# Kernel optimization log

Measured on AMD Instinct MI355X. Metric: run time of the kernel, lower is better.

Reference implementation:

```python
import jax, jax.numpy as jnp
import numpy as np

N = 100000
E = 3200000
F_IN, F1, F2, F3, FB, NC = 256, 64, 32, 16, 8, 10


def setup_inputs() -> dict:
    key = jax.random.key(0)
    ks = jax.random.split(key, 12)
    features = jax.random.normal(ks[0], (N, F_IN), dtype=jnp.float32)
    edge_index = jax.random.randint(ks[1], (2, E), 0, N, dtype=jnp.int64)
    def glorot(k, shape):
        lim = np.sqrt(6.0 / (shape[0] + shape[1]))
        return jax.random.uniform(k, shape, jnp.float32, -lim, lim)
    return {
        "features": features,
        "edge_index": edge_index,
        "W1": glorot(ks[2], (F_IN, F1)), "b1": jnp.zeros((F1,), jnp.float32),
        "W2": glorot(ks[3], (F1, F2)),  "b2": jnp.zeros((F2,), jnp.float32),
        "W3": glorot(ks[4], (F2, F3)),  "b3": jnp.zeros((F3,), jnp.float32),
        "Wf": glorot(ks[5], (F3, FB)),  "bf": jnp.zeros((FB,), jnp.float32),
        "Ws": glorot(ks[6], (FB, NC)),  "bs": jnp.zeros((NC,), jnp.float32),
    }


def _gcn_norm(edge_index, n):
    # symmetric normalization with self-loops: deg includes +1 for self-loop
    src, dst = edge_index[0], edge_index[1]
    ones = jnp.ones((edge_index.shape[1],), jnp.float32)
    deg = jax.ops.segment_sum(ones, dst, num_segments=n) + 1.0
    dinv = jax.lax.rsqrt(deg)
    edge_w = dinv[src] * dinv[dst]        # [E]
    self_w = dinv * dinv                   # [N], self-loop weight
    return src, dst, edge_w, self_w


def _gcn_conv(x, W, b, src, dst, edge_w, self_w, n):
    xw = x @ W                                         # [N, Fout]
    msg = xw[src] * edge_w[:, None]                    # gather + scale
    agg = jax.ops.segment_sum(msg, dst, num_segments=n)
    return agg + xw * self_w[:, None] + b


def reference(features, edge_index, W1, b1, W2, b2, W3, b3, Wf, bf, Ws, bs):
    n = features.shape[0]
    src, dst, edge_w, self_w = _gcn_norm(edge_index, n)
    h = jax.nn.relu(_gcn_conv(features, W1, b1, src, dst, edge_w, self_w, n))
    h = jax.nn.relu(_gcn_conv(h, W2, b2, src, dst, edge_w, self_w, n))
    h = jax.nn.relu(_gcn_conv(h, W3, b3, src, dst, edge_w, self_w, n))
    pooled = jnp.mean(h, axis=0, keepdims=True)        # [1, F3]
    hidden = jax.nn.relu(pooled @ Wf + bf)
    scores = hidden @ Ws + bs
    return jax.nn.log_softmax(scores, axis=1)
```

## Files before the change

### kernel.cpp

```cpp
#include <hip/hip_runtime.h>
#include <hip/hip_fp16.h>
#include <math.h>

#define TPB 256
#define BKT_SHIFT 9
#define BKT_N 512
#define NB_MAX 256
#define CHUNK 4096
#define CAP   24576
#define Y_SCALE 16.0f
#define Y_INV_SCALE (1.0f / 16.0f)

typedef short bf16x8 __attribute__((ext_vector_type(8)));
typedef float f32x4  __attribute__((ext_vector_type(4)));

static __device__ inline unsigned short f2bf(float f) {
    union { float f; unsigned u; } v; v.f = f;
    unsigned r = v.u + 0x7FFF + ((v.u >> 16) & 1);
    return (unsigned short)(r >> 16);
}

static __device__ inline unsigned char f2fp8(float x) {
    int p = __builtin_amdgcn_cvt_pk_fp8_f32(x, x, 0, false);
    return (unsigned char)(p & 0xFF);
}

static __device__ inline void acc_word(float* a, unsigned u) {
    a[0] += __builtin_amdgcn_cvt_f32_fp8(u, 0);
    a[1] += __builtin_amdgcn_cvt_f32_fp8(u, 1);
    a[2] += __builtin_amdgcn_cvt_f32_fp8(u, 2);
    a[3] += __builtin_amdgcn_cvt_f32_fp8(u, 3);
}

__global__ __launch_bounds__(256) void init_cursor(int* __restrict__ bcursor, int nbkt) {
    int t = threadIdx.x;
    if (t < nbkt) bcursor[t] = t * CAP;
}

__global__ __launch_bounds__(TPB) void bucket_scatter(
    const int* __restrict__ src, const int* __restrict__ dst,
    int* __restrict__ bcursor, unsigned int* __restrict__ packed, int E, int nbkt)
{
    __shared__ unsigned int  spk[CHUNK];
    __shared__ unsigned char sbk[CHUNK];
    __shared__ int h[NB_MAX];
    __shared__ int base[NB_MAX];
    for (int c0 = blockIdx.x * CHUNK; c0 < E; c0 += gridDim.x * CHUNK) {
        int m = min(CHUNK, E - c0);
        for (int i = threadIdx.x; i < nbkt; i += TPB) h[i] = 0;
        __syncthreads();
        for (int i = threadIdx.x; i < m; i += TPB) {
            int d = dst[c0 + i];
            int s = src[c0 + i];
            int b = d >> BKT_SHIFT;
            spk[i] = ((unsigned)(d & (BKT_N - 1)) << 17) | (unsigned)s;
            sbk[i] = (unsigned char)b;
            atomicAdd(&h[b], 1);
        }
        __syncthreads();
        for (int i = threadIdx.x; i < nbkt; i += TPB) {
            int c = h[i];
            base[i] = c ? atomicAdd(&bcursor[i], c) : 0;
            h[i] = 0;
        }
        __syncthreads();
        for (int i = threadIdx.x; i < m; i += TPB) {
            int b = sbk[i];
            int pos = base[b] + atomicAdd(&h[b], 1);
            packed[pos] = spk[i];
        }
        __syncthreads();
    }
}

__global__ __launch_bounds__(256) void bucket_offsets(
    const int* __restrict__ bcursor, int* __restrict__ boff, int nbkt, int E)
{
    int t = threadIdx.x;
    int v = (t < nbkt) ? (bcursor[t] - t * CAP) : 0;
    __shared__ int tmp[256];
    tmp[t] = v; __syncthreads();
    for (int s = 1; s < 256; s <<= 1) {
        int x = (t >= s) ? tmp[t - s] : 0;
        __syncthreads();
        tmp[t] += x;
        __syncthreads();
    }
    if (t < nbkt) boff[t] = tmp[t] - v;
    if (t == 0) boff[nbkt] = E;
}

__global__ __launch_bounds__(256) void bucket_csr(
    const unsigned int* __restrict__ packed, const int* __restrict__ boff,
    int* __restrict__ off, float* __restrict__ dinv, int* __restrict__ ssrc,
    int n, int nbkt)
{
    const int b   = blockIdx.x;
    const int e0  = boff[b];
    const int cnt = boff[b + 1] - e0;
    const int p0  = b * CAP;
    const int v0  = b << BKT_SHIFT;
    const int nv  = min(BKT_N, n - v0);
    const int t   = threadIdx.x;

    __shared__ int hist[BKT_N];
    __shared__ int cur[BKT_N];
    __shared__ int tmp[256];

    for (int i = t; i < nv; i += 256) hist[i] = 0;
    __syncthreads();
    for (int e = t; e < cnt; e += 256)
        atomicAdd(&hist[packed[p0 + e] >> 17], 1);
    __syncthreads();

    int a = (2 * t     < nv) ? hist[2 * t]     : 0;
    int c = (2 * t + 1 < nv) ? hist[2 * t + 1] : 0;
    int ps = a + c;
    tmp[t] = ps; __syncthreads();
    for (int s = 1; s < 256; s <<= 1) {
        int x = (t >= s) ? tmp[t - s] : 0;
        __syncthreads();
        tmp[t] += x;
        __syncthreads();
    }
    int ex = tmp[t] - ps;
    if (2 * t < nv) {
        cur[2 * t] = ex;
        off[v0 + 2 * t] = e0 + ex;
        dinv[v0 + 2 * t] = rsqrtf((float)a + 1.0f);
    }
    if (2 * t + 1 < nv) {
        cur[2 * t + 1] = ex + a;
        off[v0 + 2 * t + 1] = e0 + ex + a;
        dinv[v0 + 2 * t + 1] = rsqrtf((float)c + 1.0f);
    }
    if (b == nbkt - 1 && t == 0) off[n] = boff[nbkt];
    __syncthreads();

    for (int e = t; e < cnt; e += 256) {
        unsigned p = packed[p0 + e];
        int dl = p >> 17;
        int s  = p & 0x1FFFF;
        int pos = atomicAdd(&cur[dl], 1);
        ssrc[e0 + pos] = s;
    }
}

__global__ __launch_bounds__(256) void conv_w(
    const float* __restrict__ W, unsigned short* __restrict__ Wt, int K, int N)
{
    int total = K * N;
    for (int i = threadIdx.x + blockIdx.x * 256; i < total; i += gridDim.x * 256) {
        int k = i / N, c = i % N;
        Wt[c * K + k] = f2bf(W[i]);
    }
}

template<int K, int NCOL, typename AT>
__global__ __launch_bounds__(TPB) void gemm_mfma(
    const AT* __restrict__ A, const unsigned short* __restrict__ Wt,
    const float* __restrict__ dinv, unsigned char* __restrict__ Yq, int n)
{
    constexpr int NT = NCOL / 16;
    constexpr int KS = K / 32;
    const int lane = threadIdx.x & 63;
    const int w    = threadIdx.x >> 6;
    const int rowbase = blockIdx.x * 128 + w * 32;
    const int arow = lane & 15;
    const int kb   = (lane >> 4) * 8;

    f32x4 acc[2][NT];
#pragma unroll
    for (int mt = 0; mt < 2; mt++)
#pragma unroll
        for (int nt = 0; nt < NT; nt++) acc[mt][nt] = (f32x4)(0.f);

#pragma unroll
    for (int ks = 0; ks < KS; ks++) {
        bf16x8 a[2];
#pragma unroll
        for (int mt = 0; mt < 2; mt++) {
            int r = rowbase + mt * 16 + arow;
            if constexpr (sizeof(AT) == 4) {
                if (r < n) {
                    const float4* p = (const float4*)(A + (size_t)r * K + ks * 32 + kb);
                    float4 u = p[0], v = p[1];
                    a[mt][0] = f2bf(u.x); a[mt][1] = f2bf(u.y);
                    a[mt][2] = f2bf(u.z); a[mt][3] = f2bf(u.w);
                    a[mt][4] = f2bf(v.x); a[mt][5] = f2bf(v.y);
                    a[mt][6] = f2bf(v.z); a[mt][7] = f2bf(v.w);
                } else {
#pragma unroll
                    for (int i = 0; i < 8; i++) a[mt][i] = 0;
                }
            } else {
                if (r < n)
                    a[mt] = *(const bf16x8*)(A + (size_t)r * K + ks * 32 + kb);
                else {
#pragma unroll
                    for (int i = 0; i < 8; i++) a[mt][i] = 0;
                }
            }
        }
        bf16x8 b[NT];
#pragma unroll
        for (int nt = 0; nt < NT; nt++)
            b[nt] = *(const bf16x8*)(Wt + (size_t)(nt * 16 + arow) * K + ks * 32 + kb);
#pragma unroll
        for (int mt = 0; mt < 2; mt++)
#pragma unroll
            for (int nt = 0; nt < NT; nt++)
                acc[mt][nt] = __builtin_amdgcn_mfma_f32_16x16x32_bf16(
                    a[mt], b[nt], acc[mt][nt], 0, 0, 0);
    }

#pragma unroll
    for (int mt = 0; mt < 2; mt++) {
        int r0 = rowbase + mt * 16 + (lane >> 4) * 4;
#pragma unroll
        for (int j = 0; j < 4; j++) {
            int r = r0 + j;
            if (r < n) {
                float dv = dinv[r] * Y_SCALE;
#pragma unroll
                for (int nt = 0; nt < NT; nt++)
                    Yq[(size_t)r * NCOL + nt * 16 + arow] = f2fp8(acc[mt][nt][j] * dv);
            }
        }
    }
}

template<int F>
__global__ __launch_bounds__(TPB) void seg_group(
    const int* __restrict__ off, const int* __restrict__ ssrc,
    const unsigned char* __restrict__ Yq, const float* __restrict__ dinv,
    const float* __restrict__ bias, unsigned int* __restrict__ H, int n)
{
    constexpr int G     = F / 16;
    constexpr int LOG2G = (G == 4) ? 2 : 1;
    const int lane  = threadIdx.x & 63;
    const int fl    = lane & (G - 1);
    const int gbase = lane & ~(G - 1);
    const int v     = (blockIdx.x * TPB + threadIdx.x) >> LOG2G;

    if (v >= n) return;

    float acc[16];
#pragma unroll
    for (int i = 0; i < 16; i++) acc[i] = 0.f;

    {
        uint4 q = *(const uint4*)(Yq + (size_t)v * F + fl * 16);
        acc_word(acc + 0, q.x); acc_word(acc + 4, q.y);
        acc_word(acc + 8, q.z); acc_word(acc + 12, q.w);
    }

    const int e0 = off[v], e1 = off[v + 1];
    int e = e0;
    for (; e + G <= e1; e += G) {
        int idx = ssrc[e + fl];
        uint4 q[G];
#pragma unroll
        for (int k = 0; k < G; k++) {
            int sj = __shfl(idx, gbase + k, 64);
            q[k] = *(const uint4*)(Yq + (size_t)sj * F + fl * 16);
        }
#pragma unroll
        for (int k = 0; k < G; k++) {
            acc_word(acc + 0, q[k].x); acc_word(acc + 4, q[k].y);
            acc_word(acc + 8, q[k].z); acc_word(acc + 12, q[k].w);
        }
    }
    int rem = e1 - e;
    if (rem > 0) {
        int idx = (fl < rem) ? ssrc[e + fl] : 0;
        for (int k = 0; k < rem; k++) {
            int sj = __shfl(idx, gbase + k, 64);
            uint4 q = *(const uint4*)(Yq + (size_t)sj * F + fl * 16);
            acc_word(acc + 0, q.x); acc_word(acc + 4, q.y);
            acc_word(acc + 8, q.z); acc_word(acc + 12, q.w);
        }
    }

    float dv = dinv[v] * Y_INV_SCALE;
    unsigned hw[8];
#pragma unroll
    for (int i = 0; i < 16; i += 2) {
        float rx = fmaxf(fmaf(acc[i],     dv, bias[fl * 16 + i]),     0.f);
        float ry = fmaxf(fmaf(acc[i + 1], dv, bias[fl * 16 + i + 1]), 0.f);
        hw[i / 2] = ((unsigned)f2bf(ry) << 16) | (unsigned)f2bf(rx);
    }
    unsigned int* hp = H + (size_t)v * (F / 2) + fl * 8;
    *(uint4*)(hp + 0) = make_uint4(hw[0], hw[1], hw[2], hw[3]);
    *(uint4*)(hp + 4) = make_uint4(hw[4], hw[5], hw[6], hw[7]);
}

__global__ __launch_bounds__(TPB) void seg_pool16(
    const int* __restrict__ off, const int* __restrict__ ssrc,
    const unsigned char* __restrict__ Yq, const float* __restrict__ dinv,
    const float* __restrict__ bias, float* __restrict__ pooled, int n)
{
    constexpr int U = 4;
    const int v = blockIdx.x * TPB + threadIdx.x;

    float r16[16];
#pragma unroll
    for (int i = 0; i < 16; i++) r16[i] = 0.f;

    if (v < n) {
        float acc[16];
#pragma unroll
        for (int i = 0; i < 16; i++) acc[i] = 0.f;

        {
            uint4 q = *(const uint4*)(Yq + (size_t)v * 16);
            acc_word(acc + 0, q.x); acc_word(acc + 4, q.y);
            acc_word(acc + 8, q.z); acc_word(acc + 12, q.w);
        }
        int e0 = off[v], e1 = off[v + 1];
        int e = e0;
        for (; e + U <= e1; e += U) {
            uint4 q[U];
#pragma unroll
            for (int k = 0; k < U; k++)
                q[k] = *(const uint4*)(Yq + (size_t)ssrc[e + k] * 16);
#pragma unroll
            for (int k = 0; k < U; k++) {
                acc_word(acc + 0, q[k].x); acc_word(acc + 4, q[k].y);
                acc_word(acc + 8, q[k].z); acc_word(acc + 12, q[k].w);
            }
        }
        for (; e < e1; e++) {
            uint4 q = *(const uint4*)(Yq + (size_t)ssrc[e] * 16);
            acc_word(acc + 0, q.x); acc_word(acc + 4, q.y);
            acc_word(acc + 8, q.z); acc_word(acc + 12, q.w);
        }

        float dv = dinv[v] * Y_INV_SCALE;
#pragma unroll
        for (int i = 0; i < 16; i++)
            r16[i] = fmaxf(fmaf(acc[i], dv, bias[i]), 0.f);
    }

    __shared__ float red[TPB][17];
#pragma unroll
    for (int i = 0; i < 16; i++) red[threadIdx.x][i] = r16[i];
    __syncthreads();
    for (int st = 128; st >= 1; st >>= 1) {
        if (threadIdx.x < st) {
#pragma unroll
            for (int i = 0; i < 16; i++)
                red[threadIdx.x][i] += red[threadIdx.x + st][i];
        }
        __syncthreads();
    }
    if (threadIdx.x < 16) atomicAdd(&pooled[threadIdx.x], red[0][threadIdx.x]);
}

__global__ void head_kernel(const float* __restrict__ pooled,
                            const float* __restrict__ Wf, const float* __restrict__ bf,
                            const float* __restrict__ Ws, const float* __restrict__ bs,
                            float* __restrict__ out, float invn)
{
    if (threadIdx.x == 0 && blockIdx.x == 0) {
        float p[16], h[8], s[10];
        for (int i = 0; i < 16; i++) p[i] = pooled[i] * invn;
        for (int j = 0; j < 8; j++) {
            float a = bf[j];
            for (int i = 0; i < 16; i++) a = fmaf(p[i], Wf[i * 8 + j], a);
            h[j] = fmaxf(a, 0.f);
        }
        float m = -1e30f;
        for (int c = 0; c < 10; c++) {
            float a = bs[c];
            for (int j = 0; j < 8; j++) a = fmaf(h[j], Ws[j * 10 + c], a);
            s[c] = a;
            m = fmaxf(m, a);
        }
        float lse = 0.f;
        for (int c = 0; c < 10; c++) lse += expf(s[c] - m);
        lse = logf(lse) + m;
        for (int c = 0; c < 10; c++) out[c] = s[c] - lse;
    }
}

static inline size_t align_up(size_t x) { return (x + 255) & ~(size_t)255; }

extern "C" void kernel_launch(void* const* d_in, const int* in_sizes, int n_in,
                              void* d_out, int out_size, void* d_ws, size_t ws_size,
                              hipStream_t stream)
{
    const float* X  = (const float*)d_in[0];
    const int*   ei = (const int*)  d_in[1];
    const float* W1 = (const float*)d_in[2];  const float* b1 = (const float*)d_in[3];
    const float* W2 = (const float*)d_in[4];  const float* b2 = (const float*)d_in[5];
    const float* W3 = (const float*)d_in[6];  const float* b3 = (const float*)d_in[7];
    const float* Wf = (const float*)d_in[8];  const float* bf = (const float*)d_in[9];
    const float* Ws = (const float*)d_in[10]; const float* bs = (const float*)d_in[11];

    const int n = in_sizes[0] / 256;
    const int E = in_sizes[1] / 2;
    const int* src = ei;
    const int* dst = ei + E;
    const int nbkt = (n + BKT_N - 1) / BKT_N;

    char* ws = (char*)d_ws;
    size_t off_b = 0;
    int* bcursor = (int*)(ws + off_b);   off_b += align_up(NB_MAX * 4);
    int* boff    = (int*)(ws + off_b);   off_b += align_up((NB_MAX + 1) * 4);
    float* dinv  = (float*)(ws + off_b); off_b += align_up((size_t)n * 4);
    int* off     = (int*)(ws + off_b);   off_b += align_up((size_t)(n + 1) * 4);
    float* pooled= (float*)(ws + off_b); off_b += align_up(16 * 4);
    unsigned short* Wt1 = (unsigned short*)(ws + off_b); off_b += align_up(64 * 256 * 2);
    unsigned short* Wt2 = (unsigned short*)(ws + off_b); off_b += align_up(32 * 64 * 2);
    unsigned short* Wt3 = (unsigned short*)(ws + off_b); off_b += align_up(16 * 32 * 2);
    unsigned int* packed = (unsigned int*)(ws + off_b); off_b += align_up((size_t)nbkt * CAP * 4);
    int* ssrc    = (int*)(ws + off_b);   off_b += align_up((size_t)E * 4);
    unsigned char* Yq = (unsigned char*)(ws + off_b); off_b += align_up((size_t)n * 64);
    unsigned int* H = (unsigned int*)(ws + off_b); off_b += align_up((size_t)n * 64 * 2);

    hipMemsetAsync(pooled, 0, 16 * 4, stream);

    init_cursor<<<1, 256, 0, stream>>>(bcursor, nbkt);
    int nchunk = (E + CHUNK - 1) / CHUNK;
    bucket_scatter<<<nchunk, TPB, 0, stream>>>(src, dst, bcursor, packed, E, nbkt);
    bucket_offsets<<<1, 256, 0, stream>>>(bcursor, boff, nbkt, E);
    bucket_csr<<<nbkt, 256, 0, stream>>>(packed, boff, off, dinv, ssrc, n, nbkt);

    conv_w<<<16, 256, 0, stream>>>(W1, Wt1, 256, 64);
    conv_w<<<2, 256, 0, stream>>>(W2, Wt2, 64, 32);
    conv_w<<<1, 256, 0, stream>>>(W3, Wt3, 32, 16);

    const int gblk = (n + 127) / 128;
    const int nblk = (n + TPB - 1) / TPB;

    gemm_mfma<256, 64, float><<<gblk, TPB, 0, stream>>>(X, Wt1, dinv, Yq, n);
    seg_group<64><<<(4 * n + TPB - 1) / TPB, TPB, 0, stream>>>(off, ssrc, Yq, dinv, b1, H, n);

    gemm_mfma<64, 32, unsigned short><<<gblk, TPB, 0, stream>>>(
        (const unsigned short*)H, Wt2, dinv, Yq, n);
    seg_group<32><<<(2 * n + TPB - 1) / TPB, TPB, 0, stream>>>(off, ssrc, Yq, dinv, b2, H, n);

    gemm_mfma<32, 16, unsigned short><<<gblk, TPB, 0, stream>>>(
        (const unsigned short*)H, Wt3, dinv, Yq, n);
    seg_pool16<<<nblk, TPB, 0, stream>>>(off, ssrc, Yq, dinv, b3, pooled, n);

    head_kernel<<<1, 64, 0, stream>>>(pooled, Wf, bf, Ws, bs, (float*)d_out, 1.0f / (float)n);
}
```

Baseline: 265.0 us.

## Split layer-1 fp8 features into two column halves and aggregate each separately

The first GEMM now writes its 64-column fp8 output as two planar 32-byte-per-row halves, and the layer-1 aggregation runs as two passes of a 2-lane-per-node kernel, one per half, each writing into its slice of H. Each gather pass touches a 3.2 MB table instead of a 6.4 MB one, aiming for better cache hit rates on the random source gathers. The cost is reading the CSR offsets and indices twice plus an extra launch. The bucket-scatter chunk size is also halved.

Result: slower. 303.7 us (+14.6%).

```diff
diff --git a/kernel.cpp b/kernel.cpp
--- a/kernel.cpp
+++ b/kernel.cpp
@@ -6,7 +6,7 @@
 #define BKT_SHIFT 9
 #define BKT_N 512
 #define NB_MAX 256
-#define CHUNK 4096
+#define CHUNK 2048
 #define CAP   24576
 #define Y_SCALE 16.0f
 #define Y_INV_SCALE (1.0f / 16.0f)
@@ -222,26 +222,31 @@
             int r = r0 + j;
             if (r < n) {
                 float dv = dinv[r] * Y_SCALE;
-#pragma unroll
-                for (int nt = 0; nt < NT; nt++)
-                    Yq[(size_t)r * NCOL + nt * 16 + arow] = f2fp8(acc[mt][nt][j] * dv);
+                if constexpr (NCOL == 64) {
+#pragma unroll
+                    for (int nt = 0; nt < NT; nt++)
+                        Yq[(size_t)(nt >> 1) * n * 32 + (size_t)r * 32 +
+                           (nt & 1) * 16 + arow] = f2fp8(acc[mt][nt][j] * dv);
+                } else {
+#pragma unroll
+                    for (int nt = 0; nt < NT; nt++)
+                        Yq[(size_t)r * NCOL + nt * 16 + arow] = f2fp8(acc[mt][nt][j] * dv);
+                }
             }
         }
     }
 }
 
-template<int F>
-__global__ __launch_bounds__(TPB) void seg_group(
+template<int HSTRIDE>
+__global__ __launch_bounds__(TPB) void seg_group32(
     const int* __restrict__ off, const int* __restrict__ ssrc,
-    const unsigned char* __restrict__ Yq, const float* __restrict__ dinv,
-    const float* __restrict__ bias, unsigned int* __restrict__ H, int n)
-{
-    constexpr int G     = F / 16;
-    constexpr int LOG2G = (G == 4) ? 2 : 1;
+    const unsigned char* __restrict__ yb, const float* __restrict__ dinv,
+    const float* __restrict__ bias, unsigned int* __restrict__ H, int hoff, int n)
+{
     const int lane  = threadIdx.x & 63;
-    const int fl    = lane & (G - 1);
-    const int gbase = lane & ~(G - 1);
-    const int v     = (blockIdx.x * TPB + threadIdx.x) >> LOG2G;
+    const int fl    = lane & 1;
+    const int gbase = lane & ~1;
+    const int v     = (blockIdx.x * TPB + threadIdx.x) >> 1;
 
     if (v >= n) return;
 
@@ -250,36 +255,30 @@
     for (int i = 0; i < 16; i++) acc[i] = 0.f;
 
     {
-        uint4 q = *(const uint4*)(Yq + (size_t)v * F + fl * 16);
+        uint4 q = *(const uint4*)(yb + (size_t)v * 32 + fl * 16);
         acc_word(acc + 0, q.x); acc_word(acc + 4, q.y);
         acc_word(acc + 8, q.z); acc_word(acc + 12, q.w);
     }
 
     const int e0 = off[v], e1 = off[v + 1];
     int e = e0;
-    for (; e + G <= e1; e += G) {
+    for (; e + 2 <= e1; e += 2) {
         int idx = ssrc[e + fl];
-        uint4 q[G];
-#pragma unroll
-        for (int k = 0; k < G; k++) {
-            int sj = __shfl(idx, gbase + k, 64);
-            q[k] = *(const uint4*)(Yq + (size_t)sj * F + fl * 16);
-        }
-#pragma unroll
-        for (int k = 0; k < G; k++) {
-            acc_word(acc + 0, q[k].x); acc_word(acc + 4, q[k].y);
-            acc_word(acc + 8, q[k].z); acc_word(acc + 12, q[k].w);
-        }
-    }
-    int rem = e1 - e;
-    if (rem > 0) {
-        int idx = (fl < rem) ? ssrc[e + fl] : 0;
-        for (int k = 0; k < rem; k++) {
-            int sj = __shfl(idx, gbase + k, 64);
-            uint4 q = *(const uint4*)(Yq + (size_t)sj * F + fl * 16);
-            acc_word(acc + 0, q.x); acc_word(acc + 4, q.y);
-            acc_word(acc + 8, q.z); acc_word(acc + 12, q.w);
-        }
+        int s0 = __shfl(idx, gbase, 64);
+        int s1 = __shfl(idx, gbase + 1, 64);
+        uint4 q0 = *(const uint4*)(yb + (size_t)s0 * 32 + fl * 16);
+        uint4 q1 = *(const uint4*)(yb + (size_t)s1 * 32 + fl * 16);
+        acc_word(acc + 0, q0.x); acc_word(acc + 4, q0.y);
+        acc_word(acc + 8, q0.z); acc_word(acc + 12, q0.w);
+        acc_word(acc + 0, q1.x); acc_word(acc + 4, q1.y);
+        acc_word(acc + 8, q1.z); acc_word(acc + 12, q1.w);
+    }
+    if (e < e1) {
+        int idx = (fl == 0) ? ssrc[e] : 0;
+        int s0 = __shfl(idx, gbase, 64);
+        uint4 q = *(const uint4*)(yb + (size_t)s0 * 32 + fl * 16);
+        acc_word(acc + 0, q.x); acc_word(acc + 4, q.y);
+        acc_word(acc + 8, q.z); acc_word(acc + 12, q.w);
     }
 
     float dv = dinv[v] * Y_INV_SCALE;
@@ -290,7 +289,7 @@
         float ry = fmaxf(fmaf(acc[i + 1], dv, bias[fl * 16 + i + 1]), 0.f);
         hw[i / 2] = ((unsigned)f2bf(ry) << 16) | (unsigned)f2bf(rx);
     }
-    unsigned int* hp = H + (size_t)v * (F / 2) + fl * 8;
+    unsigned int* hp = H + (size_t)v * HSTRIDE + hoff + fl * 8;
     *(uint4*)(hp + 0) = make_uint4(hw[0], hw[1], hw[2], hw[3]);
     *(uint4*)(hp + 4) = make_uint4(hw[4], hw[5], hw[6], hw[7]);
 }
@@ -433,13 +432,15 @@
 
     const int gblk = (n + 127) / 128;
     const int nblk = (n + TPB - 1) / TPB;
+    const int sblk = (2 * n + TPB - 1) / TPB;
 
     gemm_mfma<256, 64, float><<<gblk, TPB, 0, stream>>>(X, Wt1, dinv, Yq, n);
-    seg_group<64><<<(4 * n + TPB - 1) / TPB, TPB, 0, stream>>>(off, ssrc, Yq, dinv, b1, H, n);
+    seg_group32<32><<<sblk, TPB, 0, stream>>>(off, ssrc, Yq,                dinv, b1,      H, 0,  n);
+    seg_group32<32><<<sblk, TPB, 0, stream>>>(off, ssrc, Yq + (size_t)n*32, dinv, b1 + 32, H, 16, n);
 
     gemm_mfma<64, 32, unsigned short><<<gblk, TPB, 0, stream>>>(
         (const unsigned short*)H, Wt2, dinv, Yq, n);
-    seg_group<32><<<(2 * n + TPB - 1) / TPB, TPB, 0, stream>>>(off, ssrc, Yq, dinv, b2, H, n);
+    seg_group32<16><<<sblk, TPB, 0, stream>>>(off, ssrc, Yq, dinv, b2, H, 0, n);
 
     gemm_mfma<32, 16, unsigned short><<<gblk, TPB, 0, stream>>>(
         (const unsigned short*)H, Wt3, dinv, Yq, n);
```
